# Optimization experiments

Hardware: AMD Instinct MI355X
Metric: run time of the kernel (lower is better)

Reference implementation:

```python
import jax, jax.numpy as jnp
import numpy as np

HC = 4           # hc_mult
ITERS = 20       # hc_sinkhorn_iters
EPS = 1e-6       # hc_eps
NORM_EPS = 1e-6  # rms_norm_eps


def setup_inputs() -> dict:
    key = jax.random.key(0)
    k = jax.random.split(key, 4)
    B, S, H = 1, 4096, 4096
    mix = (2 + HC) * HC  # 24
    hidden_states = jax.random.normal(k[0], (B, S, HC, H), jnp.float32)
    hc_fn = jax.random.normal(k[1], (mix, HC * H), jnp.float32) * 0.02
    hc_base = jax.random.normal(k[2], (mix,), jnp.float32) * 0.02
    hc_scale = jnp.ones((3,), jnp.float32)
    norm_weight = jnp.ones((H,), jnp.float32)
    w_inner = jax.random.normal(k[3], (H, H), jnp.float32) * 0.02
    return {
        "hidden_states": hidden_states,
        "hc_fn": hc_fn,
        "hc_base": hc_base,
        "hc_scale": hc_scale,
        "norm_weight": norm_weight,
        "w_inner": w_inner,
    }


def reference(hidden_states, hc_fn, hc_base, hc_scale, norm_weight, w_inner):
    B, S, hc, H = hidden_states.shape
    # RMS stat over the flattened (hc*H) feature dim
    flat = hidden_states.reshape(B, S, hc * H).astype(jnp.float32)
    rs = jax.lax.rsqrt(jnp.mean(jnp.square(flat), axis=-1, keepdims=True) + NORM_EPS)
    mixes = jnp.einsum('bsd,md->bsm', flat, hc_fn) * rs  # [B,S,(2+hc)*hc]

    ps, qs, cs = hc_scale[0], hc_scale[1], hc_scale[2]
    pre = jax.nn.sigmoid(mixes[..., :hc] * ps + hc_base[:hc]) + EPS           # [B,S,hc]
    post = jax.nn.sigmoid(mixes[..., hc:2 * hc] * qs + hc_base[hc:2 * hc]) + EPS
    comb = jax.nn.sigmoid(
        mixes[..., 2 * hc:].reshape(B, S, hc, hc) * cs
        + hc_base[2 * hc:].reshape(hc, hc)
    ) + EPS  # [B,S,hc,hc]

    # 20-iter Sinkhorn row/column normalization
    def sink(_, c):
        c = c / (jnp.sum(c, axis=-1, keepdims=True) + EPS)
        return c / (jnp.sum(c, axis=-2, keepdims=True) + EPS)
    comb = jax.lax.fori_loop(0, ITERS, sink, comb)

    # weighted stream reduction -> [B,S,H]
    reduced = jnp.einsum('bsh,bshd->bsd', pre, hidden_states)

    # norm + inner sub-block (RMSNorm then dense projection)
    nr = jax.lax.rsqrt(jnp.mean(jnp.square(reduced), axis=-1, keepdims=True) + NORM_EPS)
    normed = reduced * nr * norm_weight
    out = jnp.einsum('bsd,ed->bse', normed, w_inner)  # [B,S,H]

    # broadcast back to streams: post-gated write + Sinkhorn-mixed residual
    expanded = post[..., None] * out[:, :, None, :] \
        + jnp.einsum('bshk,bskd->bshd', comb, hidden_states)
    return expanded.astype(hidden_states.dtype)
```

## Files before the change

kernel.cpp:

```cpp
#include <hip/hip_runtime.h>
#include <math.h>

#define S_DIM 4096
#define H_DIM 4096
#define HC_N 4
#define HD_DIM 16384
#define MIXN 24
#define SINK_IT 20

typedef float f32x4 __attribute__((ext_vector_type(4)));
typedef __bf16 bf16x8 __attribute__((ext_vector_type(8)));
typedef unsigned short u16x8 __attribute__((ext_vector_type(8)));
typedef unsigned short u16x4 __attribute__((ext_vector_type(4)));

__device__ __forceinline__ unsigned short f2bf(float f) {
  unsigned u = __builtin_bit_cast(unsigned, f);
  u += 0x7FFFu + ((u >> 16) & 1u);
  return (unsigned short)(u >> 16);
}
__device__ __forceinline__ float bf2f(unsigned short h) {
  return __builtin_bit_cast(float, (unsigned)h << 16);
}

__global__ __launch_bounds__(256) void k_w2bf(const float* __restrict__ w,
                                              unsigned short* __restrict__ wb) {
  const size_t i = (size_t)(blockIdx.x * 256 + threadIdx.x) * 8;
  f32x4 a = *(const f32x4*)(w + i);
  f32x4 b = *(const f32x4*)(w + i + 4);
  u16x8 o;
  o[0] = f2bf(a.x); o[1] = f2bf(a.y); o[2] = f2bf(a.z); o[3] = f2bf(a.w);
  o[4] = f2bf(b.x); o[5] = f2bf(b.y); o[6] = f2bf(b.z); o[7] = f2bf(b.w);
  *(u16x8*)(wb + i) = o;
}

__global__ __launch_bounds__(256) void k_mixes(const float* __restrict__ hs,
                                               const float* __restrict__ fn,
                                               float* __restrict__ mixraw,
                                               float* __restrict__ sumsq) {
  __shared__ __align__(16) float lds[HC_N][1024];
  const int tid = threadIdx.x;
  const int b = blockIdx.x;
  const int lane = tid & 63, wave = tid >> 6;
  const int mbase = wave * 6;

  float acc[HC_N][6];
  float ss[HC_N];
#pragma unroll
  for (int r = 0; r < HC_N; r++) {
    ss[r] = 0.f;
#pragma unroll
    for (int j = 0; j < 6; j++) acc[r][j] = 0.f;
  }

  const size_t rowbase = (size_t)b * HC_N * HD_DIM;
  for (int it = 0; it < 16; ++it) {
    __syncthreads();
#pragma unroll
    for (int r = 0; r < HC_N; r++) {
      f32x4 v = *(const f32x4*)(hs + rowbase + (size_t)r * HD_DIM + it * 1024 + tid * 4);
      *(f32x4*)(&lds[r][tid * 4]) = v;
    }
    __syncthreads();
#pragma unroll
    for (int ii = 0; ii < 4; ii++) {
      const int c4 = ii * 64 + lane;
      f32x4 h4[HC_N];
#pragma unroll
      for (int r = 0; r < HC_N; r++) h4[r] = *(const f32x4*)(&lds[r][c4 * 4]);
      if (wave == 0) {
#pragma unroll
        for (int r = 0; r < HC_N; r++)
          ss[r] += h4[r].x * h4[r].x + h4[r].y * h4[r].y + h4[r].z * h4[r].z + h4[r].w * h4[r].w;
      }
#pragma unroll
      for (int j = 0; j < 6; j++) {
        f32x4 fv = *(const f32x4*)(fn + (size_t)(mbase + j) * HD_DIM + it * 1024 + c4 * 4);
#pragma unroll
        for (int r = 0; r < HC_N; r++)
          acc[r][j] += h4[r].x * fv.x + h4[r].y * fv.y + h4[r].z * fv.z + h4[r].w * fv.w;
      }
    }
  }

#pragma unroll
  for (int r = 0; r < HC_N; r++) {
#pragma unroll
    for (int j = 0; j < 6; j++) {
      float v = acc[r][j];
#pragma unroll
      for (int off = 32; off >= 1; off >>= 1) v += __shfl_xor(v, off, 64);
      if (lane == 0) mixraw[(size_t)(b * 4 + r) * MIXN + mbase + j] = v;
    }
  }
  if (wave == 0) {
#pragma unroll
    for (int r = 0; r < HC_N; r++) {
      float v = ss[r];
#pragma unroll
      for (int off = 32; off >= 1; off >>= 1) v += __shfl_xor(v, off, 64);
      if (lane == 0) sumsq[b * 4 + r] = v;
    }
  }
}

__global__ __launch_bounds__(256) void k_gates(const float* __restrict__ mixraw,
                                               const float* __restrict__ sumsq,
                                               const float* __restrict__ hbase,
                                               const float* __restrict__ hscale,
                                               float* __restrict__ gates) {
  const int row = blockIdx.x * 256 + threadIdx.x;
  const float rs = rsqrtf(sumsq[row] * (1.0f / HD_DIM) + 1e-6f);
  const float ps = hscale[0], qs = hscale[1], cs = hscale[2];
  const float* mr = mixraw + (size_t)row * MIXN;
  float g[MIXN];
#pragma unroll
  for (int m = 0; m < MIXN; m++) {
    const float sc = (m < 4) ? ps : ((m < 8) ? qs : cs);
    const float x = mr[m] * rs * sc + hbase[m];
    g[m] = 1.0f / (1.0f + expf(-x)) + 1e-6f;
  }
  for (int t = 0; t < SINK_IT; t++) {
#pragma unroll
    for (int i = 0; i < 4; i++) {
      const float s = g[8 + i * 4 + 0] + g[8 + i * 4 + 1] + g[8 + i * 4 + 2] + g[8 + i * 4 + 3] + 1e-6f;
#pragma unroll
      for (int j = 0; j < 4; j++) g[8 + i * 4 + j] /= s;
    }
#pragma unroll
    for (int j = 0; j < 4; j++) {
      const float s = g[8 + 0 + j] + g[8 + 4 + j] + g[8 + 8 + j] + g[8 + 12 + j] + 1e-6f;
#pragma unroll
      for (int i = 0; i < 4; i++) g[8 + i * 4 + j] /= s;
    }
  }
  float* go = gates + (size_t)row * MIXN;
#pragma unroll
  for (int m = 0; m < MIXN; m++) go[m] = g[m];
}

__global__ __launch_bounds__(256) void k_reduce_norm(const float* __restrict__ hs,
                                                     const float* __restrict__ gates,
                                                     const float* __restrict__ nw,
                                                     unsigned short* __restrict__ normed) {
  const int s = blockIdx.x, tid = threadIdx.x;
  const int lane = tid & 63, wave = tid >> 6;
  const float* g = gates + (size_t)s * MIXN;
  const float p0 = g[0], p1 = g[1], p2 = g[2], p3 = g[3];
  const size_t base = (size_t)s * HC_N * H_DIM;

  f32x4 red[4];
  float ssq = 0.f;
#pragma unroll
  for (int it = 0; it < 4; ++it) {
    const int d4 = it * 256 + tid;
    f32x4 a = *(const f32x4*)(hs + base + (size_t)0 * H_DIM + (size_t)d4 * 4);
    f32x4 b = *(const f32x4*)(hs + base + (size_t)1 * H_DIM + (size_t)d4 * 4);
    f32x4 c = *(const f32x4*)(hs + base + (size_t)2 * H_DIM + (size_t)d4 * 4);
    f32x4 d = *(const f32x4*)(hs + base + (size_t)3 * H_DIM + (size_t)d4 * 4);
    f32x4 v = p0 * a + p1 * b + p2 * c + p3 * d;
    red[it] = v;
    ssq += v.x * v.x + v.y * v.y + v.z * v.z + v.w * v.w;
  }
#pragma unroll
  for (int off = 32; off >= 1; off >>= 1) ssq += __shfl_xor(ssq, off, 64);
  __shared__ float ls[4];
  if (lane == 0) ls[wave] = ssq;
  __syncthreads();
  const float tot = ls[0] + ls[1] + ls[2] + ls[3];
  const float nr = rsqrtf(tot * (1.0f / H_DIM) + 1e-6f);
#pragma unroll
  for (int it = 0; it < 4; ++it) {
    const int d4 = it * 256 + tid;
    f32x4 w = *(const f32x4*)(nw + (size_t)d4 * 4);
    f32x4 v = red[it] * nr;
    v = v * w;
    u16x4 o;
    o[0] = f2bf(v.x); o[1] = f2bf(v.y); o[2] = f2bf(v.z); o[3] = f2bf(v.w);
    *(u16x4*)(normed + (size_t)s * H_DIM + (size_t)d4 * 4) = o;
  }
}

__device__ __forceinline__ void gload_lds16(const unsigned short* g, unsigned short* l) {
  __builtin_amdgcn_global_load_lds(
      (const __attribute__((address_space(1))) unsigned int*)(const void*)g,
      (__attribute__((address_space(3))) unsigned int*)(void*)l, 16, 0, 0);
}

__global__ __launch_bounds__(256) void k_gemm(const unsigned short* __restrict__ A,
                                              const unsigned short* __restrict__ B,
                                              unsigned short* __restrict__ C) {
  __shared__ __align__(16) unsigned short sA[128 * 32];
  __shared__ __align__(16) unsigned short sB[128 * 32];
  const int tid = threadIdx.x;
  const int lane = tid & 63, wave = tid >> 6;
  const int bm = blockIdx.y, bn = blockIdx.x;
  const int wm = wave >> 1, wn = wave & 1;

  f32x4 zero = {0.f, 0.f, 0.f, 0.f};
  f32x4 acc[4][4];
#pragma unroll
  for (int mi = 0; mi < 4; mi++)
#pragma unroll
    for (int ni = 0; ni < 4; ni++) acc[mi][ni] = zero;

  const int strow = lane >> 2;
  const int stk = (lane & 3) * 8;
  const unsigned short* ga = A + (size_t)(bm * 128) * 4096;
  const unsigned short* gb = B + (size_t)(bn * 128) * 4096;
  const int c0 = wave * 2, c1 = wave * 2 + 1;

  for (int kk = 0; kk < 4096; kk += 32) {
    gload_lds16(ga + (size_t)(c0 * 16 + strow) * 4096 + kk + stk, sA + c0 * 512);
    gload_lds16(ga + (size_t)(c1 * 16 + strow) * 4096 + kk + stk, sA + c1 * 512);
    gload_lds16(gb + (size_t)(c0 * 16 + strow) * 4096 + kk + stk, sB + c0 * 512);
    gload_lds16(gb + (size_t)(c1 * 16 + strow) * 4096 + kk + stk, sB + c1 * 512);
    __syncthreads();

    const int rb = lane & 15, kq = (lane >> 4) * 8;
    bf16x8 af[4], bfr[4];
#pragma unroll
    for (int mi = 0; mi < 4; mi++)
      af[mi] = *(const bf16x8*)(sA + (wm * 64 + mi * 16 + rb) * 32 + kq);
#pragma unroll
    for (int ni = 0; ni < 4; ni++)
      bfr[ni] = *(const bf16x8*)(sB + (wn * 64 + ni * 16 + rb) * 32 + kq);
#pragma unroll
    for (int mi = 0; mi < 4; mi++)
#pragma unroll
      for (int ni = 0; ni < 4; ni++)
        acc[mi][ni] = __builtin_amdgcn_mfma_f32_16x16x32_bf16(af[mi], bfr[ni], acc[mi][ni], 0, 0, 0);
    __syncthreads();
  }

  const int cr = (lane >> 4) * 4, cc = lane & 15;
#pragma unroll
  for (int mi = 0; mi < 4; mi++)
#pragma unroll
    for (int ni = 0; ni < 4; ni++)
#pragma unroll
      for (int j = 0; j < 4; j++) {
        const int row = bm * 128 + wm * 64 + mi * 16 + cr + j;
        const int col = bn * 128 + wn * 64 + ni * 16 + cc;
        C[(size_t)row * 4096 + col] = f2bf(acc[mi][ni][j]);
      }
}

__global__ __launch_bounds__(256) void k_expand(const float* __restrict__ hs,
                                                const unsigned short* __restrict__ outb,
                                                const float* __restrict__ gates,
                                                float* __restrict__ y) {
  const int s = blockIdx.x, tid = threadIdx.x;
  const float* g = gates + (size_t)s * MIXN;
  float post[4], cb[4][4];
#pragma unroll
  for (int h = 0; h < 4; h++) post[h] = g[4 + h];
#pragma unroll
  for (int h = 0; h < 4; h++)
#pragma unroll
    for (int k = 0; k < 4; k++) cb[h][k] = g[8 + h * 4 + k];

  const size_t base = (size_t)s * HC_N * H_DIM;
#pragma unroll
  for (int it = 0; it < 4; ++it) {
    const int d4 = it * 256 + tid;
    f32x4 hv[4];
#pragma unroll
    for (int k = 0; k < 4; k++)
      hv[k] = *(const f32x4*)(hs + base + (size_t)k * H_DIM + (size_t)d4 * 4);
    u16x4 ob = *(const u16x4*)(outb + (size_t)s * H_DIM + (size_t)d4 * 4);
    f32x4 o = {bf2f(ob[0]), bf2f(ob[1]), bf2f(ob[2]), bf2f(ob[3])};
#pragma unroll
    for (int h = 0; h < 4; h++) {
      f32x4 e = post[h] * o + cb[h][0] * hv[0] + cb[h][1] * hv[1] + cb[h][2] * hv[2] + cb[h][3] * hv[3];
      *(f32x4*)(y + base + (size_t)h * H_DIM + (size_t)d4 * 4) = e;
    }
  }
}

extern "C" void kernel_launch(void* const* d_in, const int* in_sizes, int n_in,
                              void* d_out, int out_size, void* d_ws, size_t ws_size,
                              hipStream_t stream) {
  const float* hs = (const float*)d_in[0];
  const float* fn = (const float*)d_in[1];
  const float* hbase = (const float*)d_in[2];
  const float* hscale = (const float*)d_in[3];
  const float* nw = (const float*)d_in[4];
  const float* wi = (const float*)d_in[5];
  float* y = (float*)d_out;

  char* ws = (char*)d_ws;
  float* mixraw = (float*)(ws);
  float* sumsq = (float*)(ws + 393216);
  float* gates = (float*)(ws + 409600);
  unsigned short* normed = (unsigned short*)(ws + 1048576);
  unsigned short* wb = (unsigned short*)(ws + 1048576 + 33554432);
  unsigned short* outb = (unsigned short*)(ws + 1048576 + 2 * 33554432);

  k_w2bf<<<8192, 256, 0, stream>>>(wi, wb);
  k_mixes<<<1024, 256, 0, stream>>>(hs, fn, mixraw, sumsq);
  k_gates<<<16, 256, 0, stream>>>(mixraw, sumsq, hbase, hscale, gates);
  k_reduce_norm<<<4096, 256, 0, stream>>>(hs, gates, nw, normed);
  k_gemm<<<dim3(32, 32), 256, 0, stream>>>(normed, wb, outb);
  k_expand<<<4096, 256, 0, stream>>>(hs, outb, gates, y);
}
```

Measured before the change: 490.1 us.

## Rewrite bf16 GEMM with 256x256 tiles and 4-stage async LDS pipeline

```diff
diff --git a/kernel.cpp b/kernel.cpp
--- a/kernel.cpp
+++ b/kernel.cpp
@@ -186,63 +186,93 @@
       (__attribute__((address_space(3))) unsigned int*)(void*)l, 16, 0, 0);
 }
 
-__global__ __launch_bounds__(256) void k_gemm(const unsigned short* __restrict__ A,
-                                              const unsigned short* __restrict__ B,
-                                              unsigned short* __restrict__ C) {
-  __shared__ __align__(16) unsigned short sA[128 * 32];
-  __shared__ __align__(16) unsigned short sB[128 * 32];
+#define GEMM_NT 128
+
+__global__ __launch_bounds__(512, 2) void k_gemm(const unsigned short* __restrict__ A,
+                                                 const unsigned short* __restrict__ B,
+                                                 unsigned short* __restrict__ C) {
+  __shared__ __align__(16) unsigned short sA[4][256 * 32];
+  __shared__ __align__(16) unsigned short sB[4][256 * 32];
   const int tid = threadIdx.x;
   const int lane = tid & 63, wave = tid >> 6;
-  const int bm = blockIdx.y, bn = blockIdx.x;
-  const int wm = wave >> 1, wn = wave & 1;
-
+
+  const int bid = blockIdx.x;
+  const int v = bid & 7, u = bid >> 3;
+  const int bm = u & 15, bn = v * 2 + (u >> 4);
+  const int wm = wave >> 2, wn = wave & 3;
+
+  const int srow = lane >> 2;
+  const int sk = (lane & 3) * 8;
+  const unsigned short* ga = A + (size_t)(bm * 256 + wave * 32 + srow) * 4096 + sk;
+  const unsigned short* gb = B + (size_t)(bn * 256 + wave * 32 + srow) * 4096 + sk;
+  const int ldst0 = wave * 1024 + lane * 8;
+  const int ldst1 = ldst0 + 512;
+
+#define STAGE(slot, t) do {                                        \
+    const unsigned short* gha = ga + (size_t)(t) * 32;             \
+    const unsigned short* ghb = gb + (size_t)(t) * 32;             \
+    gload_lds16(gha,             &sA[(slot)][ldst0]);              \
+    gload_lds16(gha + 16 * 4096, &sA[(slot)][ldst1]);              \
+    gload_lds16(ghb,             &sB[(slot)][ldst0]);              \
+    gload_lds16(ghb + 16 * 4096, &sB[(slot)][ldst1]);              \
+  } while (0)
+
+  f32x4 acc[8][4];
   f32x4 zero = {0.f, 0.f, 0.f, 0.f};
-  f32x4 acc[4][4];
-#pragma unroll
-  for (int mi = 0; mi < 4; mi++)
-#pragma unroll
-    for (int ni = 0; ni < 4; ni++) acc[mi][ni] = zero;
-
-  const int strow = lane >> 2;
-  const int stk = (lane & 3) * 8;
-  const unsigned short* ga = A + (size_t)(bm * 128) * 4096;
-  const unsigned short* gb = B + (size_t)(bn * 128) * 4096;
-  const int c0 = wave * 2, c1 = wave * 2 + 1;
-
-  for (int kk = 0; kk < 4096; kk += 32) {
-    gload_lds16(ga + (size_t)(c0 * 16 + strow) * 4096 + kk + stk, sA + c0 * 512);
-    gload_lds16(ga + (size_t)(c1 * 16 + strow) * 4096 + kk + stk, sA + c1 * 512);
-    gload_lds16(gb + (size_t)(c0 * 16 + strow) * 4096 + kk + stk, sB + c0 * 512);
-    gload_lds16(gb + (size_t)(c1 * 16 + strow) * 4096 + kk + stk, sB + c1 * 512);
-    __syncthreads();
-
-    const int rb = lane & 15, kq = (lane >> 4) * 8;
-    bf16x8 af[4], bfr[4];
-#pragma unroll
-    for (int mi = 0; mi < 4; mi++)
-      af[mi] = *(const bf16x8*)(sA + (wm * 64 + mi * 16 + rb) * 32 + kq);
-#pragma unroll
-    for (int ni = 0; ni < 4; ni++)
-      bfr[ni] = *(const bf16x8*)(sB + (wn * 64 + ni * 16 + rb) * 32 + kq);
-#pragma unroll
-    for (int mi = 0; mi < 4; mi++)
-#pragma unroll
-      for (int ni = 0; ni < 4; ni++)
-        acc[mi][ni] = __builtin_amdgcn_mfma_f32_16x16x32_bf16(af[mi], bfr[ni], acc[mi][ni], 0, 0, 0);
-    __syncthreads();
-  }
-
-  const int cr = (lane >> 4) * 4, cc = lane & 15;
-#pragma unroll
-  for (int mi = 0; mi < 4; mi++)
-#pragma unroll
-    for (int ni = 0; ni < 4; ni++)
-#pragma unroll
-      for (int j = 0; j < 4; j++) {
-        const int row = bm * 128 + wm * 64 + mi * 16 + cr + j;
-        const int col = bn * 128 + wn * 64 + ni * 16 + cc;
-        C[(size_t)row * 4096 + col] = f2bf(acc[mi][ni][j]);
-      }
+#pragma unroll
+  for (int mf = 0; mf < 8; mf++)
+#pragma unroll
+    for (int nf = 0; nf < 4; nf++) acc[mf][nf] = zero;
+
+  const int frow = lane & 15, fk = (lane >> 4) * 8;
+  const int abase = wm * 128 + frow;
+  const int bbase = wn * 64 + frow;
+
+#define COMPUTE(slot) do {                                                    \
+    bf16x8 af[8], bfr[4];                                                     \
+    _Pragma("unroll") for (int mf = 0; mf < 8; mf++)                          \
+      af[mf] = *(const bf16x8*)&sA[(slot)][(abase + mf * 16) * 32 + fk];      \
+    _Pragma("unroll") for (int nf = 0; nf < 4; nf++)                          \
+      bfr[nf] = *(const bf16x8*)&sB[(slot)][(bbase + nf * 16) * 32 + fk];     \
+    __builtin_amdgcn_s_setprio(1);                                            \
+    _Pragma("unroll") for (int mf = 0; mf < 8; mf++)                          \
+      _Pragma("unroll") for (int nf = 0; nf < 4; nf++)                        \
+        acc[mf][nf] = __builtin_amdgcn_mfma_f32_16x16x32_bf16(af[mf], bfr[nf], acc[mf][nf], 0, 0, 0); \
+    __builtin_amdgcn_s_setprio(0);                                            \
+  } while (0)
+
+  STAGE(0, 0);
+  STAGE(1, 1);
+  STAGE(2, 2);
+  asm volatile("s_waitcnt vmcnt(8)" ::: "memory");
+  asm volatile("s_barrier" ::: "memory");
+
+  for (int t = 0; t < GEMM_NT - 3; ++t) {
+    STAGE((t + 3) & 3, t + 3);
+    COMPUTE(t & 3);
+    asm volatile("s_waitcnt vmcnt(8)" ::: "memory");
+    asm volatile("s_barrier" ::: "memory");
+  }
+  COMPUTE((GEMM_NT - 3) & 3);
+  asm volatile("s_waitcnt vmcnt(4)" ::: "memory");
+  asm volatile("s_barrier" ::: "memory");
+  COMPUTE((GEMM_NT - 2) & 3);
+  asm volatile("s_waitcnt vmcnt(0)" ::: "memory");
+  asm volatile("s_barrier" ::: "memory");
+  COMPUTE((GEMM_NT - 1) & 3);
+
+#undef STAGE
+#undef COMPUTE
+
+  const int crow0 = bm * 256 + wm * 128 + (lane >> 4) * 4;
+  const int ccol0 = bn * 256 + wn * 64 + (lane & 15);
+#pragma unroll
+  for (int mf = 0; mf < 8; mf++)
+#pragma unroll
+    for (int nf = 0; nf < 4; nf++)
+#pragma unroll
+      for (int j = 0; j < 4; j++)
+        C[(size_t)(crow0 + mf * 16 + j) * 4096 + ccol0 + nf * 16] = f2bf(acc[mf][nf][j]);
 }
 
 __global__ __launch_bounds__(256) void k_expand(const float* __restrict__ hs,
@@ -300,6 +330,6 @@
   k_mixes<<<1024, 256, 0, stream>>>(hs, fn, mixraw, sumsq);
   k_gates<<<16, 256, 0, stream>>>(mixraw, sumsq, hbase, hscale, gates);
   k_reduce_norm<<<4096, 256, 0, stream>>>(hs, gates, nw, normed);
-  k_gemm<<<dim3(32, 32), 256, 0, stream>>>(normed, wb, outb);
+  k_gemm<<<256, 512, 0, stream>>>(normed, wb, outb);
   k_expand<<<4096, 256, 0, stream>>>(hs, outb, gates, y);
 }
```

Result: no change. 487.1 us (-0.6%).

## Double-buffer mixes LDS staging, prefetch fn rows, swizzle GEMM LDS layout

Applied to the files above, without the earlier changes.

```diff
diff --git a/kernel.cpp b/kernel.cpp
--- a/kernel.cpp
+++ b/kernel.cpp
@@ -37,7 +37,7 @@
                                                const float* __restrict__ fn,
                                                float* __restrict__ mixraw,
                                                float* __restrict__ sumsq) {
-  __shared__ __align__(16) float lds[HC_N][1024];
+  __shared__ __align__(16) float lds[2][HC_N][1024];
   const int tid = threadIdx.x;
   const int b = blockIdx.x;
   const int lane = tid & 63, wave = tid >> 6;
@@ -53,20 +53,41 @@
   }
 
   const size_t rowbase = (size_t)b * HC_N * HD_DIM;
+
+#pragma unroll
+  for (int r = 0; r < HC_N; r++) {
+    f32x4 v = *(const f32x4*)(hs + rowbase + (size_t)r * HD_DIM + tid * 4);
+    *(f32x4*)(&lds[0][r][tid * 4]) = v;
+  }
+  __syncthreads();
+
   for (int it = 0; it < 16; ++it) {
-    __syncthreads();
-#pragma unroll
-    for (int r = 0; r < HC_N; r++) {
-      f32x4 v = *(const f32x4*)(hs + rowbase + (size_t)r * HD_DIM + it * 1024 + tid * 4);
-      *(f32x4*)(&lds[r][tid * 4]) = v;
-    }
-    __syncthreads();
+    const int cur = it & 1;
+    f32x4 nx[HC_N];
+    if (it + 1 < 16) {
+#pragma unroll
+      for (int r = 0; r < HC_N; r++)
+        nx[r] = *(const f32x4*)(hs + rowbase + (size_t)r * HD_DIM + (it + 1) * 1024 + tid * 4);
+    }
+    f32x4 fvp[6];
+#pragma unroll
+    for (int j = 0; j < 6; j++)
+      fvp[j] = *(const f32x4*)(fn + (size_t)(mbase + j) * HD_DIM + it * 1024 + lane * 4);
+
 #pragma unroll
     for (int ii = 0; ii < 4; ii++) {
       const int c4 = ii * 64 + lane;
       f32x4 h4[HC_N];
 #pragma unroll
-      for (int r = 0; r < HC_N; r++) h4[r] = *(const f32x4*)(&lds[r][c4 * 4]);
+      for (int r = 0; r < HC_N; r++) h4[r] = *(const f32x4*)(&lds[cur][r][c4 * 4]);
+      f32x4 fv[6];
+#pragma unroll
+      for (int j = 0; j < 6; j++) fv[j] = fvp[j];
+      if (ii + 1 < 4) {
+#pragma unroll
+        for (int j = 0; j < 6; j++)
+          fvp[j] = *(const f32x4*)(fn + (size_t)(mbase + j) * HD_DIM + it * 1024 + (c4 + 64) * 4);
+      }
       if (wave == 0) {
 #pragma unroll
         for (int r = 0; r < HC_N; r++)
@@ -74,11 +95,17 @@
       }
 #pragma unroll
       for (int j = 0; j < 6; j++) {
-        f32x4 fv = *(const f32x4*)(fn + (size_t)(mbase + j) * HD_DIM + it * 1024 + c4 * 4);
 #pragma unroll
         for (int r = 0; r < HC_N; r++)
-          acc[r][j] += h4[r].x * fv.x + h4[r].y * fv.y + h4[r].z * fv.z + h4[r].w * fv.w;
+          acc[r][j] += h4[r].x * fv[j].x + h4[r].y * fv[j].y + h4[r].z * fv[j].z + h4[r].w * fv[j].w;
       }
+    }
+
+    if (it + 1 < 16) {
+#pragma unroll
+      for (int r = 0; r < HC_N; r++)
+        *(f32x4*)(&lds[cur ^ 1][r][tid * 4]) = nx[r];
+      __syncthreads();
     }
   }
 
@@ -186,9 +213,9 @@
       (__attribute__((address_space(3))) unsigned int*)(void*)l, 16, 0, 0);
 }
 
-__global__ __launch_bounds__(256) void k_gemm(const unsigned short* __restrict__ A,
-                                              const unsigned short* __restrict__ B,
-                                              unsigned short* __restrict__ C) {
+__global__ __launch_bounds__(256, 4) void k_gemm(const unsigned short* __restrict__ A,
+                                                 const unsigned short* __restrict__ B,
+                                                 unsigned short* __restrict__ C) {
   __shared__ __align__(16) unsigned short sA[128 * 32];
   __shared__ __align__(16) unsigned short sB[128 * 32];
   const int tid = threadIdx.x;
@@ -204,10 +231,13 @@
     for (int ni = 0; ni < 4; ni++) acc[mi][ni] = zero;
 
   const int strow = lane >> 2;
-  const int stk = (lane & 3) * 8;
+  const int stk = (((lane & 3) ^ ((lane >> 3) & 3)) * 8);
   const unsigned short* ga = A + (size_t)(bm * 128) * 4096;
   const unsigned short* gb = B + (size_t)(bn * 128) * 4096;
   const int c0 = wave * 2, c1 = wave * 2 + 1;
+
+  const int rb = lane & 15;
+  const int fk = (((lane >> 4) ^ ((lane >> 1) & 3)) * 8);
 
   for (int kk = 0; kk < 4096; kk += 32) {
     gload_lds16(ga + (size_t)(c0 * 16 + strow) * 4096 + kk + stk, sA + c0 * 512);
@@ -216,14 +246,13 @@
     gload_lds16(gb + (size_t)(c1 * 16 + strow) * 4096 + kk + stk, sB + c1 * 512);
     __syncthreads();
 
-    const int rb = lane & 15, kq = (lane >> 4) * 8;
     bf16x8 af[4], bfr[4];
 #pragma unroll
     for (int mi = 0; mi < 4; mi++)
-      af[mi] = *(const bf16x8*)(sA + (wm * 64 + mi * 16 + rb) * 32 + kq);
+      af[mi] = *(const bf16x8*)(sA + (wm * 64 + mi * 16 + rb) * 32 + fk);
 #pragma unroll
     for (int ni = 0; ni < 4; ni++)
-      bfr[ni] = *(const bf16x8*)(sB + (wn * 64 + ni * 16 + rb) * 32 + kq);
+      bfr[ni] = *(const bf16x8*)(sB + (wn * 64 + ni * 16 + rb) * 32 + fk);
 #pragma unroll
     for (int mi = 0; mi < 4; mi++)
 #pragma unroll
```

Result: faster. 457.7 us (-6.6%).
